# Kernel optimization log

Hardware: AMD Instinct MI355X
Metric: run time of the kernel (lower is better)

The kernel has to match this reference:

```python
import jax, jax.numpy as jnp
import numpy as np

THR = 0.2
BORDER_RM = 2
TEMP = 0.1


def _border_valid(n, b):
    idx = jnp.arange(n)
    return (idx >= b) & (idx < n - b)


def setup_inputs() -> dict:
    key = jax.random.key(0)
    k0, k1 = jax.random.split(key)
    N, L, S, C = 4, 3600, 3600, 256
    return {
        "feat_c0": jax.random.normal(k0, (N, L, C), dtype=jnp.float32),
        "feat_c1": jax.random.normal(k1, (N, S, C), dtype=jnp.float32),
        "h0c": 60, "w0c": 60, "h1c": 60, "w1c": 60,
    }


def reference(feat_c0, feat_c1, h0c, w0c, h1c, w1c):
    N, L, C = feat_c0.shape
    S = feat_c1.shape[1]
    inv_sqrt_c = 1.0 / (C ** 0.5)
    f0 = feat_c0 * inv_sqrt_c
    f1 = feat_c1 * inv_sqrt_c
    # [N, L, S] similarity, temperature 0.1
    sim = jnp.einsum('nlc,nsc->nls', f0, f1) / TEMP
    conf = jax.nn.softmax(sim, axis=1) * jax.nn.softmax(sim, axis=2)

    # threshold mask + border removal (applied in [b,h0,w0,h1,w1] layout,
    # expressed here as separable 1D validity masks -- same result, no 5D copy churn)
    v0h = _border_valid(h0c, BORDER_RM)  # [h0c]
    v0w = _border_valid(w0c, BORDER_RM)
    v1h = _border_valid(h1c, BORDER_RM)
    v1w = _border_valid(w1c, BORDER_RM)
    valid_l = (v0h[:, None] & v0w[None, :]).reshape(L)   # [L]
    valid_s = (v1h[:, None] & v1w[None, :]).reshape(S)   # [S]
    mask = (conf > THR) & valid_l[None, :, None] & valid_s[None, None, :]

    # mutual nearest (dual argmax equality)
    mask = mask & (conf == conf.max(axis=2, keepdims=True)) & (conf == conf.max(axis=1, keepdims=True))

    # fixed-shape match extraction: per (b, i) row, is there a match and where
    mask_v = jnp.any(mask, axis=2)                       # [N, L] bool
    all_j_ids = jnp.argmax(mask, axis=2)                 # [N, L] int
    mconf = jnp.take_along_axis(conf, all_j_ids[:, :, None], axis=2)[:, :, 0]
    mconf = jnp.where(mask_v, mconf, 0.0)                # [N, L]
    return conf, mask_v, all_j_ids, mconf
```

## Files before the change

### kernel.cpp

```cpp
#include <hip/hip_runtime.h>
#include <stdint.h>


typedef _Float16 f16;
typedef _Float16 f16x8 __attribute__((ext_vector_type(8)));
typedef _Float16 f16x4 __attribute__((ext_vector_type(4)));
typedef float f32x4 __attribute__((ext_vector_type(4)));

#define N_B 4
#define L_DIM 3600
#define S_DIM 3600
#define C_DIM 256

#define P1_THREADS 192
#define P1_BM 144
#define P1_BN 48
#define P1_ITERS 15
#define P1_CHUNK 720
#define P1_NCH 5
#define P1_NRT 25
#define YT_STRIDE 264

#define P2_ROWS 48
#define P2_NRT 75

#define C_EXP1 (0.0390625f * 1.4426950408889634f)

__global__ void cast_kernel(const float* __restrict__ a, const float* __restrict__ b,
                            f16* __restrict__ ah, f16* __restrict__ bh, int total8) {
  int i = blockIdx.x * blockDim.x + threadIdx.x;
  if (i >= total8) return;
  const float4* a4 = (const float4*)a;
  const float4* b4 = (const float4*)b;
  float4 x = a4[2 * (size_t)i], y = a4[2 * (size_t)i + 1];
  f16x8 o = {(f16)x.x, (f16)x.y, (f16)x.z, (f16)x.w,
             (f16)y.x, (f16)y.y, (f16)y.z, (f16)y.w};
  *(f16x8*)(ah + 8 * (size_t)i) = o;
  x = b4[2 * (size_t)i]; y = b4[2 * (size_t)i + 1];
  f16x8 o2 = {(f16)x.x, (f16)x.y, (f16)x.z, (f16)x.w,
              (f16)y.x, (f16)y.y, (f16)y.z, (f16)y.w};
  *(f16x8*)(bh + 8 * (size_t)i) = o2;
}

__global__ __launch_bounds__(P1_THREADS) void gemm_stats_kernel(
    const f16* __restrict__ X, const f16* __restrict__ Y,
    f16* __restrict__ eh, float* __restrict__ den_r, float* __restrict__ den_c) {
  __shared__ f16 Yt[P1_BN][YT_STRIDE];
  __shared__ float colsum_w[3][P1_CHUNK];
  const int rt = blockIdx.x, ch = blockIdx.y, n = blockIdx.z;
  const int tid = threadIdx.x;
  const int wave = tid >> 6, lane = tid & 63;
  const int q = lane >> 4, r = lane & 15;
  const int l0 = rt * P1_BM;
  const int s0 = ch * P1_CHUNK;

  f16x8 a[3][8];
#pragma unroll
  for (int grp = 0; grp < 3; ++grp) {
    const f16* xrow = X + ((size_t)n * L_DIM + l0 + wave * 48 + grp * 16 + r) * C_DIM;
#pragma unroll
    for (int k = 0; k < 8; ++k) a[grp][k] = *(const f16x8*)(xrow + k * 32 + q * 8);
  }

  float sum_e[3][4];
#pragma unroll
  for (int grp = 0; grp < 3; ++grp)
#pragma unroll
    for (int g = 0; g < 4; ++g) sum_e[grp][g] = 0.f;

  const f16* ebase = eh + ((size_t)n * L_DIM + l0 + wave * 48) * S_DIM;

  for (int it = 0; it < P1_ITERS; ++it) {
    const f16* ysrc = Y + ((size_t)n * S_DIM + s0 + it * P1_BN) * C_DIM;
#pragma unroll
    for (int i = 0; i < 8; ++i) {
      int c = i * P1_THREADS + tid;
      int row = c >> 5, cc = c & 31;
      *(f16x8*)&Yt[row][cc * 8] = *(const f16x8*)(ysrc + row * C_DIM + cc * 8);
    }
    __syncthreads();

    f32x4 acc[3][3];
#pragma unroll
    for (int grp = 0; grp < 3; ++grp)
#pragma unroll
      for (int nt = 0; nt < 3; ++nt) acc[grp][nt] = (f32x4){0.f, 0.f, 0.f, 0.f};

#pragma unroll
    for (int k = 0; k < 8; ++k) {
#pragma unroll
      for (int nt = 0; nt < 3; ++nt) {
        f16x8 b = *(const f16x8*)&Yt[nt * 16 + r][k * 32 + q * 8];
#pragma unroll
        for (int grp = 0; grp < 3; ++grp)
          acc[grp][nt] = __builtin_amdgcn_mfma_f32_16x16x32_f16(a[grp][k], b, acc[grp][nt], 0, 0, 0);
      }
    }
    __syncthreads();

#pragma unroll
    for (int nt = 0; nt < 3; ++nt) {
      int scol = s0 + it * P1_BN + nt * 16 + r;
      float csum = 0.f;
#pragma unroll
      for (int grp = 0; grp < 3; ++grp) {
#pragma unroll
        for (int g = 0; g < 4; ++g) {
          float e = exp2f(acc[grp][nt][g] * C_EXP1);
          sum_e[grp][g] += e;
          csum += e;
          ((f16*)ebase)[(size_t)(grp * 16 + q * 4 + g) * S_DIM + scol] = (f16)e;
        }
      }
      csum += __shfl_xor(csum, 16, 64);
      csum += __shfl_xor(csum, 32, 64);
      if (q == 0) colsum_w[wave][it * P1_BN + nt * 16 + r] = csum;
    }
  }

#pragma unroll
  for (int m = 1; m < 16; m <<= 1)
#pragma unroll
    for (int grp = 0; grp < 3; ++grp)
#pragma unroll
      for (int g = 0; g < 4; ++g) sum_e[grp][g] += __shfl_xor(sum_e[grp][g], m, 64);
  if (r == 0) {
#pragma unroll
    for (int grp = 0; grp < 3; ++grp)
#pragma unroll
      for (int g = 0; g < 4; ++g)
        atomicAdd(&den_r[n * L_DIM + l0 + wave * 48 + grp * 16 + q * 4 + g], sum_e[grp][g]);
  }

  __syncthreads();
  for (int i = tid; i < P1_CHUNK; i += P1_THREADS)
    atomicAdd(&den_c[n * S_DIM + s0 + i],
              colsum_w[0][i] + colsum_w[1][i] + colsum_w[2][i]);
}

__global__ void invert_kernel(float* __restrict__ a, float* __restrict__ b) {
  int i = blockIdx.x * blockDim.x + threadIdx.x;
  if (i >= N_B * L_DIM) return;
  a[i] = 1.0f / a[i];
  b[i] = 1.0f / b[i];
}

__global__ __launch_bounds__(256) void conf_kernel(
    const f16* __restrict__ eh, const float* __restrict__ invdr,
    const float* __restrict__ invdc, float* __restrict__ conf_out,
    unsigned long long* __restrict__ rowarg, float* __restrict__ colpart) {
  const int rt = blockIdx.x, n = blockIdx.y;
  const int tid = threadIdx.x;
  const int wave = tid >> 6, lane = tid & 63;
  const int l0 = rt * P2_ROWS;

  int colb[4];
  bool cv[4];
  float4 idc4[4];
  float4 cp[4];
#pragma unroll
  for (int ci = 0; ci < 4; ++ci) {
    int chunk = ci * 64 + lane;
    cv[ci] = chunk < 225;
    colb[ci] = (wave * 225 + (chunk < 225 ? chunk : 0)) * 4;
    idc4[ci] = *(const float4*)(invdc + n * S_DIM + colb[ci]);
    cp[ci] = (float4){0.f, 0.f, 0.f, 0.f};
  }

  for (int row = 0; row < P2_ROWS; ++row) {
    const int l = l0 + row;
    const f16* erow = eh + ((size_t)n * L_DIM + l) * S_DIM;
    float* crow = conf_out + ((size_t)n * L_DIM + l) * S_DIM;
    const float idr = invdr[n * L_DIM + l];
    float mx = 0.f;
    int mj = 0;
#pragma unroll
    for (int ci = 0; ci < 4; ++ci) {
      if (cv[ci]) {
        f16x4 e4 = *(const f16x4*)(erow + colb[ci]);
        float e0 = (float)e4.x, e1 = (float)e4.y, e2 = (float)e4.z, e3 = (float)e4.w;
        float4 w;
        w.x = e0 * e0 * idr * idc4[ci].x;
        w.y = e1 * e1 * idr * idc4[ci].y;
        w.z = e2 * e2 * idr * idc4[ci].z;
        w.w = e3 * e3 * idr * idc4[ci].w;
        *(float4*)(crow + colb[ci]) = w;
        int c0 = colb[ci];
        if (w.x > mx) { mx = w.x; mj = c0; }
        if (w.y > mx) { mx = w.y; mj = c0 + 1; }
        if (w.z > mx) { mx = w.z; mj = c0 + 2; }
        if (w.w > mx) { mx = w.w; mj = c0 + 3; }
        cp[ci].x = fmaxf(cp[ci].x, w.x);
        cp[ci].y = fmaxf(cp[ci].y, w.y);
        cp[ci].z = fmaxf(cp[ci].z, w.z);
        cp[ci].w = fmaxf(cp[ci].w, w.w);
      }
    }
#pragma unroll
    for (int m = 1; m < 64; m <<= 1) {
      float ov = __shfl_xor(mx, m, 64);
      int oj = __shfl_xor(mj, m, 64);
      if (ov > mx || (ov == mx && oj < mj)) { mx = ov; mj = oj; }
    }
    if (lane == 0) {
      unsigned long long key =
          ((unsigned long long)__float_as_uint(mx) << 32) |
          (unsigned int)(~(unsigned int)mj);
      atomicMax(&rowarg[n * L_DIM + l], key);
    }
  }

  float* cpo = colpart + ((size_t)n * P2_NRT + rt) * S_DIM;
#pragma unroll
  for (int ci = 0; ci < 4; ++ci)
    if (cv[ci]) *(float4*)(cpo + colb[ci]) = cp[ci];
}

__global__ void colmerge_kernel(const float* __restrict__ colpart,
                                float* __restrict__ colmax) {
  int i = blockIdx.x * blockDim.x + threadIdx.x;
  if (i >= N_B * S_DIM) return;
  int n = i / S_DIM, s = i - n * S_DIM;
  float m = 0.f;
  for (int rt = 0; rt < P2_NRT; ++rt)
    m = fmaxf(m, colpart[((size_t)n * P2_NRT + rt) * S_DIM + s]);
  colmax[i] = m;
}

__global__ void finalize_kernel(const unsigned long long* __restrict__ rowarg,
                                const float* __restrict__ colmax,
                                const int* __restrict__ h0c, const int* __restrict__ w0c,
                                const int* __restrict__ h1c, const int* __restrict__ w1c,
                                float* __restrict__ out_maskv, float* __restrict__ out_jids,
                                float* __restrict__ out_mconf) {
  int i = blockIdx.x * blockDim.x + threadIdx.x;
  if (i >= N_B * L_DIM) return;
  int n = i / L_DIM, l = i - n * L_DIM;
  unsigned long long key = rowarg[i];
  float rm = __uint_as_float((unsigned int)(key >> 32));
  int j = (int)(~(unsigned int)key);
  int W0 = *w0c, H0 = *h0c, W1 = *w1c, H1 = *h1c;
  int li = l / W0, lj = l - li * W0;
  bool vl = (li >= 2) && (li < H0 - 2) && (lj >= 2) && (lj < W0 - 2);
  int si = j / W1, sj = j - si * W1;
  bool vs = (si >= 2) && (si < H1 - 2) && (sj >= 2) && (sj < W1 - 2);
  float cm = colmax[n * S_DIM + j];
  bool mv = (rm > 0.2f) && vl && vs &&
            (__float_as_uint(rm) == __float_as_uint(cm));
  out_maskv[i] = mv ? 1.0f : 0.0f;
  out_jids[i]  = mv ? (float)j : 0.0f;
  out_mconf[i] = mv ? rm : 0.0f;
}

extern "C" void kernel_launch(void* const* d_in, const int* in_sizes, int n_in,
                              void* d_out, int out_size, void* d_ws, size_t ws_size,
                              hipStream_t stream) {
  const float* f0 = (const float*)d_in[0];
  const float* f1 = (const float*)d_in[1];
  const int* h0c = (const int*)d_in[2];
  const int* w0c = (const int*)d_in[3];
  const int* h1c = (const int*)d_in[4];
  const int* w1c = (const int*)d_in[5];

  char* ws = (char*)d_ws;
  size_t o = 0;
  f16* f0h = (f16*)(ws + o);               o += (size_t)N_B * L_DIM * C_DIM * 2;
  f16* f1h = (f16*)(ws + o);               o += (size_t)N_B * S_DIM * C_DIM * 2;
  float* den_r = (float*)(ws + o);         o += (size_t)N_B * L_DIM * 4;
  float* den_c = (float*)(ws + o);         o += (size_t)N_B * S_DIM * 4;
  unsigned long long* rowarg = (unsigned long long*)(ws + o); o += (size_t)N_B * L_DIM * 8;
  size_t zero_bytes = (size_t)N_B * L_DIM * (4 + 4 + 8);
  float* colmax = (float*)(ws + o);        o += (size_t)N_B * S_DIM * 4;
  float* colpart = (float*)(ws + o);       o += (size_t)N_B * P2_NRT * S_DIM * 4;
  f16* eh = (f16*)(ws + o);                o += (size_t)N_B * L_DIM * S_DIM * 2;

  float* conf = (float*)d_out;
  float* out_maskv = conf + (size_t)N_B * L_DIM * S_DIM;
  float* out_jids = out_maskv + N_B * L_DIM;
  float* out_mconf = out_jids + N_B * L_DIM;

  hipMemsetAsync(den_r, 0, zero_bytes, stream);

  int total8 = N_B * L_DIM * C_DIM / 8;
  cast_kernel<<<dim3((total8 + 255) / 256), 256, 0, stream>>>(f0, f1, f0h, f1h, total8);

  dim3 g1(P1_NRT, P1_NCH, N_B);
  gemm_stats_kernel<<<g1, P1_THREADS, 0, stream>>>(f0h, f1h, eh, den_r, den_c);
  invert_kernel<<<(N_B * L_DIM + 255) / 256, 256, 0, stream>>>(den_r, den_c);
  dim3 g2(P2_NRT, N_B);
  conf_kernel<<<g2, 256, 0, stream>>>(eh, den_r, den_c, conf, rowarg, colpart);
  colmerge_kernel<<<(N_B * S_DIM + 255) / 256, 256, 0, stream>>>(colpart, colmax);
  finalize_kernel<<<(N_B * L_DIM + 255) / 256, 256, 0, stream>>>(
      rowarg, colmax, h0c, w0c, h1c, w1c, out_maskv, out_jids, out_mconf);
}
```

Baseline: 416.7 us.

## Recompute GEMM in conf pass instead of storing fp16 exp matrix

```diff
diff --git a/kernel.cpp b/kernel.cpp
--- a/kernel.cpp
+++ b/kernel.cpp
@@ -4,7 +4,6 @@
 
 typedef _Float16 f16;
 typedef _Float16 f16x8 __attribute__((ext_vector_type(8)));
-typedef _Float16 f16x4 __attribute__((ext_vector_type(4)));
 typedef float f32x4 __attribute__((ext_vector_type(4)));
 
 #define N_B 4
@@ -21,10 +20,8 @@
 #define P1_NRT 25
 #define YT_STRIDE 264
 
-#define P2_ROWS 48
-#define P2_NRT 75
-
 #define C_EXP1 (0.0390625f * 1.4426950408889634f)
+#define C_EXP2 (0.0781250f * 1.4426950408889634f)
 
 __global__ void cast_kernel(const float* __restrict__ a, const float* __restrict__ b,
                             f16* __restrict__ ah, f16* __restrict__ bh, int total8) {
@@ -44,7 +41,7 @@
 
 __global__ __launch_bounds__(P1_THREADS) void gemm_stats_kernel(
     const f16* __restrict__ X, const f16* __restrict__ Y,
-    f16* __restrict__ eh, float* __restrict__ den_r, float* __restrict__ den_c) {
+    float* __restrict__ den_r, float* __restrict__ den_c) {
   __shared__ f16 Yt[P1_BN][YT_STRIDE];
   __shared__ float colsum_w[3][P1_CHUNK];
   const int rt = blockIdx.x, ch = blockIdx.y, n = blockIdx.z;
@@ -68,8 +65,6 @@
 #pragma unroll
     for (int g = 0; g < 4; ++g) sum_e[grp][g] = 0.f;
 
-  const f16* ebase = eh + ((size_t)n * L_DIM + l0 + wave * 48) * S_DIM;
-
   for (int it = 0; it < P1_ITERS; ++it) {
     const f16* ysrc = Y + ((size_t)n * S_DIM + s0 + it * P1_BN) * C_DIM;
 #pragma unroll
@@ -100,7 +95,6 @@
 
 #pragma unroll
     for (int nt = 0; nt < 3; ++nt) {
-      int scol = s0 + it * P1_BN + nt * 16 + r;
       float csum = 0.f;
 #pragma unroll
       for (int grp = 0; grp < 3; ++grp) {
@@ -109,7 +103,6 @@
           float e = exp2f(acc[grp][nt][g] * C_EXP1);
           sum_e[grp][g] += e;
           csum += e;
-          ((f16*)ebase)[(size_t)(grp * 16 + q * 4 + g) * S_DIM + scol] = (f16)e;
         }
       }
       csum += __shfl_xor(csum, 16, 64);
@@ -145,86 +138,121 @@
   b[i] = 1.0f / b[i];
 }
 
-__global__ __launch_bounds__(256) void conf_kernel(
-    const f16* __restrict__ eh, const float* __restrict__ invdr,
-    const float* __restrict__ invdc, float* __restrict__ conf_out,
-    unsigned long long* __restrict__ rowarg, float* __restrict__ colpart) {
-  const int rt = blockIdx.x, n = blockIdx.y;
+__global__ __launch_bounds__(P1_THREADS) void gemm_conf_kernel(
+    const f16* __restrict__ X, const f16* __restrict__ Y,
+    const float* __restrict__ invdr, const float* __restrict__ invdc,
+    float* __restrict__ conf_out,
+    unsigned long long* __restrict__ rowarg,
+    unsigned int* __restrict__ colmax_bits) {
+  __shared__ f16 Yt[P1_BN][YT_STRIDE];
+  __shared__ float colmax_w[3][P1_CHUNK];
+  const int rt = blockIdx.x, ch = blockIdx.y, n = blockIdx.z;
   const int tid = threadIdx.x;
   const int wave = tid >> 6, lane = tid & 63;
-  const int l0 = rt * P2_ROWS;
-
-  int colb[4];
-  bool cv[4];
-  float4 idc4[4];
-  float4 cp[4];
-#pragma unroll
-  for (int ci = 0; ci < 4; ++ci) {
-    int chunk = ci * 64 + lane;
-    cv[ci] = chunk < 225;
-    colb[ci] = (wave * 225 + (chunk < 225 ? chunk : 0)) * 4;
-    idc4[ci] = *(const float4*)(invdc + n * S_DIM + colb[ci]);
-    cp[ci] = (float4){0.f, 0.f, 0.f, 0.f};
-  }
-
-  for (int row = 0; row < P2_ROWS; ++row) {
-    const int l = l0 + row;
-    const f16* erow = eh + ((size_t)n * L_DIM + l) * S_DIM;
-    float* crow = conf_out + ((size_t)n * L_DIM + l) * S_DIM;
-    const float idr = invdr[n * L_DIM + l];
-    float mx = 0.f;
-    int mj = 0;
-#pragma unroll
-    for (int ci = 0; ci < 4; ++ci) {
-      if (cv[ci]) {
-        f16x4 e4 = *(const f16x4*)(erow + colb[ci]);
-        float e0 = (float)e4.x, e1 = (float)e4.y, e2 = (float)e4.z, e3 = (float)e4.w;
-        float4 w;
-        w.x = e0 * e0 * idr * idc4[ci].x;
-        w.y = e1 * e1 * idr * idc4[ci].y;
-        w.z = e2 * e2 * idr * idc4[ci].z;
-        w.w = e3 * e3 * idr * idc4[ci].w;
-        *(float4*)(crow + colb[ci]) = w;
-        int c0 = colb[ci];
-        if (w.x > mx) { mx = w.x; mj = c0; }
-        if (w.y > mx) { mx = w.y; mj = c0 + 1; }
-        if (w.z > mx) { mx = w.z; mj = c0 + 2; }
-        if (w.w > mx) { mx = w.w; mj = c0 + 3; }
-        cp[ci].x = fmaxf(cp[ci].x, w.x);
-        cp[ci].y = fmaxf(cp[ci].y, w.y);
-        cp[ci].z = fmaxf(cp[ci].z, w.z);
-        cp[ci].w = fmaxf(cp[ci].w, w.w);
-      }
-    }
-#pragma unroll
-    for (int m = 1; m < 64; m <<= 1) {
-      float ov = __shfl_xor(mx, m, 64);
-      int oj = __shfl_xor(mj, m, 64);
-      if (ov > mx || (ov == mx && oj < mj)) { mx = ov; mj = oj; }
-    }
-    if (lane == 0) {
-      unsigned long long key =
-          ((unsigned long long)__float_as_uint(mx) << 32) |
-          (unsigned int)(~(unsigned int)mj);
-      atomicMax(&rowarg[n * L_DIM + l], key);
-    }
-  }
-
-  float* cpo = colpart + ((size_t)n * P2_NRT + rt) * S_DIM;
-#pragma unroll
-  for (int ci = 0; ci < 4; ++ci)
-    if (cv[ci]) *(float4*)(cpo + colb[ci]) = cp[ci];
-}
-
-__global__ void colmerge_kernel(const float* __restrict__ colpart,
-                                float* __restrict__ colmax) {
-  int i = blockIdx.x * blockDim.x + threadIdx.x;
-  if (i >= N_B * S_DIM) return;
-  int n = i / S_DIM, s = i - n * S_DIM;
-  float m = 0.f;
-  for (int rt = 0; rt < P2_NRT; ++rt)
-    m = fmaxf(m, colpart[((size_t)n * P2_NRT + rt) * S_DIM + s]);
-  colmax[i] = m;
+  const int q = lane >> 4, r = lane & 15;
+  const int l0 = rt * P1_BM;
+  const int s0 = ch * P1_CHUNK;
+
+  f16x8 a[3][8];
+#pragma unroll
+  for (int grp = 0; grp < 3; ++grp) {
+    const f16* xrow = X + ((size_t)n * L_DIM + l0 + wave * 48 + grp * 16 + r) * C_DIM;
+#pragma unroll
+    for (int k = 0; k < 8; ++k) a[grp][k] = *(const f16x8*)(xrow + k * 32 + q * 8);
+  }
+
+  float idr[3][4];
+#pragma unroll
+  for (int grp = 0; grp < 3; ++grp)
+#pragma unroll
+    for (int g = 0; g < 4; ++g)
+      idr[grp][g] = invdr[n * L_DIM + l0 + wave * 48 + grp * 16 + q * 4 + g];
+
+  float mx[12];
+  int mj[12];
+#pragma unroll
+  for (int i = 0; i < 12; ++i) { mx[i] = 0.f; mj[i] = 0; }
+
+  float* cbase = conf_out + ((size_t)n * L_DIM + l0 + wave * 48) * S_DIM;
+
+  for (int it = 0; it < P1_ITERS; ++it) {
+    const f16* ysrc = Y + ((size_t)n * S_DIM + s0 + it * P1_BN) * C_DIM;
+#pragma unroll
+    for (int i = 0; i < 8; ++i) {
+      int c = i * P1_THREADS + tid;
+      int row = c >> 5, cc = c & 31;
+      *(f16x8*)&Yt[row][cc * 8] = *(const f16x8*)(ysrc + row * C_DIM + cc * 8);
+    }
+    __syncthreads();
+
+    f32x4 acc[3][3];
+#pragma unroll
+    for (int grp = 0; grp < 3; ++grp)
+#pragma unroll
+      for (int nt = 0; nt < 3; ++nt) acc[grp][nt] = (f32x4){0.f, 0.f, 0.f, 0.f};
+
+#pragma unroll
+    for (int k = 0; k < 8; ++k) {
+#pragma unroll
+      for (int nt = 0; nt < 3; ++nt) {
+        f16x8 b = *(const f16x8*)&Yt[nt * 16 + r][k * 32 + q * 8];
+#pragma unroll
+        for (int grp = 0; grp < 3; ++grp)
+          acc[grp][nt] = __builtin_amdgcn_mfma_f32_16x16x32_f16(a[grp][k], b, acc[grp][nt], 0, 0, 0);
+      }
+    }
+    __syncthreads();
+
+#pragma unroll
+    for (int nt = 0; nt < 3; ++nt) {
+      const int scol = s0 + it * P1_BN + nt * 16 + r;
+      const float idc = invdc[n * S_DIM + scol];
+      float cm = 0.f;
+#pragma unroll
+      for (int grp = 0; grp < 3; ++grp) {
+#pragma unroll
+        for (int g = 0; g < 4; ++g) {
+          float w = exp2f(acc[grp][nt][g] * C_EXP2) * idr[grp][g] * idc;
+          cbase[(size_t)(grp * 16 + q * 4 + g) * S_DIM + scol] = w;
+          const int idx = grp * 4 + g;
+          if (w > mx[idx]) { mx[idx] = w; mj[idx] = scol; }
+          cm = fmaxf(cm, w);
+        }
+      }
+      cm = fmaxf(cm, __shfl_xor(cm, 16, 64));
+      cm = fmaxf(cm, __shfl_xor(cm, 32, 64));
+      if (q == 0) colmax_w[wave][it * P1_BN + nt * 16 + r] = cm;
+    }
+  }
+
+#pragma unroll
+  for (int m = 1; m < 16; m <<= 1) {
+#pragma unroll
+    for (int idx = 0; idx < 12; ++idx) {
+      float ov = __shfl_xor(mx[idx], m, 64);
+      int oj = __shfl_xor(mj[idx], m, 64);
+      if (ov > mx[idx] || (ov == mx[idx] && oj < mj[idx])) { mx[idx] = ov; mj[idx] = oj; }
+    }
+  }
+  if (r == 0) {
+#pragma unroll
+    for (int grp = 0; grp < 3; ++grp) {
+#pragma unroll
+      for (int g = 0; g < 4; ++g) {
+        const int idx = grp * 4 + g;
+        unsigned long long key =
+            ((unsigned long long)__float_as_uint(mx[idx]) << 32) |
+            (unsigned int)(~(unsigned int)mj[idx]);
+        atomicMax(&rowarg[n * L_DIM + l0 + wave * 48 + grp * 16 + q * 4 + g], key);
+      }
+    }
+  }
+
+  __syncthreads();
+  for (int i = tid; i < P1_CHUNK; i += P1_THREADS) {
+    float m3 = fmaxf(fmaxf(colmax_w[0][i], colmax_w[1][i]), colmax_w[2][i]);
+    atomicMax(&colmax_bits[n * S_DIM + s0 + i], __float_as_uint(m3));
+  }
 }
 
 __global__ void finalize_kernel(const unsigned long long* __restrict__ rowarg,
@@ -269,10 +297,8 @@
   float* den_r = (float*)(ws + o);         o += (size_t)N_B * L_DIM * 4;
   float* den_c = (float*)(ws + o);         o += (size_t)N_B * S_DIM * 4;
   unsigned long long* rowarg = (unsigned long long*)(ws + o); o += (size_t)N_B * L_DIM * 8;
-  size_t zero_bytes = (size_t)N_B * L_DIM * (4 + 4 + 8);
   float* colmax = (float*)(ws + o);        o += (size_t)N_B * S_DIM * 4;
-  float* colpart = (float*)(ws + o);       o += (size_t)N_B * P2_NRT * S_DIM * 4;
-  f16* eh = (f16*)(ws + o);                o += (size_t)N_B * L_DIM * S_DIM * 2;
+  size_t zero_bytes = (size_t)N_B * (L_DIM * 4 + S_DIM * 4 + L_DIM * 8 + S_DIM * 4);
 
   float* conf = (float*)d_out;
   float* out_maskv = conf + (size_t)N_B * L_DIM * S_DIM;
@@ -285,11 +311,10 @@
   cast_kernel<<<dim3((total8 + 255) / 256), 256, 0, stream>>>(f0, f1, f0h, f1h, total8);
 
   dim3 g1(P1_NRT, P1_NCH, N_B);
-  gemm_stats_kernel<<<g1, P1_THREADS, 0, stream>>>(f0h, f1h, eh, den_r, den_c);
+  gemm_stats_kernel<<<g1, P1_THREADS, 0, stream>>>(f0h, f1h, den_r, den_c);
   invert_kernel<<<(N_B * L_DIM + 255) / 256, 256, 0, stream>>>(den_r, den_c);
-  dim3 g2(P2_NRT, N_B);
-  conf_kernel<<<g2, 256, 0, stream>>>(eh, den_r, den_c, conf, rowarg, colpart);
-  colmerge_kernel<<<(N_B * S_DIM + 255) / 256, 256, 0, stream>>>(colpart, colmax);
+  gemm_conf_kernel<<<g1, P1_THREADS, 0, stream>>>(
+      f0h, f1h, den_r, den_c, conf, rowarg, (unsigned int*)colmax);
   finalize_kernel<<<(N_B * L_DIM + 255) / 256, 256, 0, stream>>>(
       rowarg, colmax, h0c, w0c, h1c, w1c, out_maskv, out_jids, out_mconf);
 }
```

Measured after the change: 431.5 us. 1.04x slower.

## Transpose MFMA output for vector e stores and stream conf with LDS column max

Applied to the files above, without the earlier changes.

```diff
diff --git a/kernel.cpp b/kernel.cpp
--- a/kernel.cpp
+++ b/kernel.cpp
@@ -15,14 +15,13 @@
 #define P1_THREADS 192
 #define P1_BM 144
 #define P1_BN 48
-#define P1_ITERS 15
-#define P1_CHUNK 720
-#define P1_NCH 5
+#define P1_ITERS 5
+#define P1_CHUNK 240
+#define P1_NCH 15
 #define P1_NRT 25
 #define YT_STRIDE 264
 
-#define P2_ROWS 48
-#define P2_NRT 75
+#define PB_ROWS 16
 
 #define C_EXP1 (0.0390625f * 1.4426950408889634f)
 
@@ -42,11 +41,11 @@
   *(f16x8*)(bh + 8 * (size_t)i) = o2;
 }
 
-__global__ __launch_bounds__(P1_THREADS) void gemm_stats_kernel(
+__global__ __launch_bounds__(P1_THREADS, 2) void gemm_stats_e_kernel(
     const f16* __restrict__ X, const f16* __restrict__ Y,
     f16* __restrict__ eh, float* __restrict__ den_r, float* __restrict__ den_c) {
   __shared__ f16 Yt[P1_BN][YT_STRIDE];
-  __shared__ float colsum_w[3][P1_CHUNK];
+  __shared__ __attribute__((aligned(16))) float colsum_w[3][P1_CHUNK];
   const int rt = blockIdx.x, ch = blockIdx.y, n = blockIdx.z;
   const int tid = threadIdx.x;
   const int wave = tid >> 6, lane = tid & 63;
@@ -62,13 +61,11 @@
     for (int k = 0; k < 8; ++k) a[grp][k] = *(const f16x8*)(xrow + k * 32 + q * 8);
   }
 
-  float sum_e[3][4];
-#pragma unroll
-  for (int grp = 0; grp < 3; ++grp)
-#pragma unroll
-    for (int g = 0; g < 4; ++g) sum_e[grp][g] = 0.f;
-
-  const f16* ebase = eh + ((size_t)n * L_DIM + l0 + wave * 48) * S_DIM;
+  float prs[3];
+#pragma unroll
+  for (int grp = 0; grp < 3; ++grp) prs[grp] = 0.f;
+
+  f16* ebase = eh + ((size_t)n * L_DIM + l0 + wave * 48) * S_DIM;
 
   for (int it = 0; it < P1_ITERS; ++it) {
     const f16* ysrc = Y + ((size_t)n * S_DIM + s0 + it * P1_BN) * C_DIM;
@@ -93,43 +90,46 @@
         f16x8 b = *(const f16x8*)&Yt[nt * 16 + r][k * 32 + q * 8];
 #pragma unroll
         for (int grp = 0; grp < 3; ++grp)
-          acc[grp][nt] = __builtin_amdgcn_mfma_f32_16x16x32_f16(a[grp][k], b, acc[grp][nt], 0, 0, 0);
+          acc[grp][nt] = __builtin_amdgcn_mfma_f32_16x16x32_f16(b, a[grp][k], acc[grp][nt], 0, 0, 0);
       }
     }
     __syncthreads();
 
 #pragma unroll
     for (int nt = 0; nt < 3; ++nt) {
-      int scol = s0 + it * P1_BN + nt * 16 + r;
-      float csum = 0.f;
+      const int sl = it * P1_BN + nt * 16 + q * 4;
+      f32x4 c4 = (f32x4){0.f, 0.f, 0.f, 0.f};
 #pragma unroll
       for (int grp = 0; grp < 3; ++grp) {
-#pragma unroll
-        for (int g = 0; g < 4; ++g) {
-          float e = exp2f(acc[grp][nt][g] * C_EXP1);
-          sum_e[grp][g] += e;
-          csum += e;
-          ((f16*)ebase)[(size_t)(grp * 16 + q * 4 + g) * S_DIM + scol] = (f16)e;
-        }
-      }
-      csum += __shfl_xor(csum, 16, 64);
-      csum += __shfl_xor(csum, 32, 64);
-      if (q == 0) colsum_w[wave][it * P1_BN + nt * 16 + r] = csum;
-    }
-  }
-
-#pragma unroll
-  for (int m = 1; m < 16; m <<= 1)
+        f32x4 e4;
+        e4.x = exp2f(acc[grp][nt][0] * C_EXP1);
+        e4.y = exp2f(acc[grp][nt][1] * C_EXP1);
+        e4.z = exp2f(acc[grp][nt][2] * C_EXP1);
+        e4.w = exp2f(acc[grp][nt][3] * C_EXP1);
+        f16x4 h = {(f16)e4.x, (f16)e4.y, (f16)e4.z, (f16)e4.w};
+        *(f16x4*)(ebase + (size_t)(grp * 16 + r) * S_DIM + s0 + sl) = h;
+        prs[grp] += e4.x + e4.y + e4.z + e4.w;
+        c4.x += e4.x; c4.y += e4.y; c4.z += e4.z; c4.w += e4.w;
+      }
+#pragma unroll
+      for (int m = 1; m < 16; m <<= 1) {
+        c4.x += __shfl_xor(c4.x, m, 64);
+        c4.y += __shfl_xor(c4.y, m, 64);
+        c4.z += __shfl_xor(c4.z, m, 64);
+        c4.w += __shfl_xor(c4.w, m, 64);
+      }
+      if (r == 0) *(f32x4*)&colsum_w[wave][sl] = c4;
+    }
+  }
+
+#pragma unroll
+  for (int m = 16; m < 64; m <<= 1)
+#pragma unroll
+    for (int grp = 0; grp < 3; ++grp) prs[grp] += __shfl_xor(prs[grp], m, 64);
+  if (q == 0) {
 #pragma unroll
     for (int grp = 0; grp < 3; ++grp)
-#pragma unroll
-      for (int g = 0; g < 4; ++g) sum_e[grp][g] += __shfl_xor(sum_e[grp][g], m, 64);
-  if (r == 0) {
-#pragma unroll
-    for (int grp = 0; grp < 3; ++grp)
-#pragma unroll
-      for (int g = 0; g < 4; ++g)
-        atomicAdd(&den_r[n * L_DIM + l0 + wave * 48 + grp * 16 + q * 4 + g], sum_e[grp][g]);
+      atomicAdd(&den_r[n * L_DIM + l0 + wave * 48 + grp * 16 + r], prs[grp]);
   }
 
   __syncthreads();
@@ -145,55 +145,52 @@
   b[i] = 1.0f / b[i];
 }
 
-__global__ __launch_bounds__(256) void conf_kernel(
+__global__ __launch_bounds__(256, 4) void conf_stream_kernel(
     const f16* __restrict__ eh, const float* __restrict__ invdr,
     const float* __restrict__ invdc, float* __restrict__ conf_out,
-    unsigned long long* __restrict__ rowarg, float* __restrict__ colpart) {
-  const int rt = blockIdx.x, n = blockIdx.y;
-  const int tid = threadIdx.x;
-  const int wave = tid >> 6, lane = tid & 63;
-  const int l0 = rt * P2_ROWS;
-
-  int colb[4];
-  bool cv[4];
-  float4 idc4[4];
-  float4 cp[4];
-#pragma unroll
-  for (int ci = 0; ci < 4; ++ci) {
-    int chunk = ci * 64 + lane;
-    cv[ci] = chunk < 225;
-    colb[ci] = (wave * 225 + (chunk < 225 ? chunk : 0)) * 4;
-    idc4[ci] = *(const float4*)(invdc + n * S_DIM + colb[ci]);
-    cp[ci] = (float4){0.f, 0.f, 0.f, 0.f};
-  }
-
-  for (int row = 0; row < P2_ROWS; ++row) {
-    const int l = l0 + row;
+    unsigned long long* __restrict__ rowarg,
+    unsigned int* __restrict__ colmax_bits) {
+  __shared__ unsigned cmx_lds[S_DIM];
+  const int n = blockIdx.y;
+  const int l0 = blockIdx.x * PB_ROWS;
+  const int tid = threadIdx.x, wave = tid >> 6, lane = tid & 63;
+
+  for (int i = tid; i < S_DIM; i += 256) cmx_lds[i] = 0u;
+  __syncthreads();
+
+  f32x4 cm[15];
+#pragma unroll
+  for (int c = 0; c < 15; ++c) cm[c] = (f32x4){0.f, 0.f, 0.f, 0.f};
+
+  const float* idcb = invdc + (size_t)n * S_DIM;
+
+  for (int rr = 0; rr < 4; ++rr) {
+    const int l = l0 + wave * 4 + rr;
+    const float idr = invdr[n * L_DIM + l];
     const f16* erow = eh + ((size_t)n * L_DIM + l) * S_DIM;
     float* crow = conf_out + ((size_t)n * L_DIM + l) * S_DIM;
-    const float idr = invdr[n * L_DIM + l];
     float mx = 0.f;
     int mj = 0;
 #pragma unroll
-    for (int ci = 0; ci < 4; ++ci) {
-      if (cv[ci]) {
-        f16x4 e4 = *(const f16x4*)(erow + colb[ci]);
-        float e0 = (float)e4.x, e1 = (float)e4.y, e2 = (float)e4.z, e3 = (float)e4.w;
-        float4 w;
-        w.x = e0 * e0 * idr * idc4[ci].x;
-        w.y = e1 * e1 * idr * idc4[ci].y;
-        w.z = e2 * e2 * idr * idc4[ci].z;
-        w.w = e3 * e3 * idr * idc4[ci].w;
-        *(float4*)(crow + colb[ci]) = w;
-        int c0 = colb[ci];
-        if (w.x > mx) { mx = w.x; mj = c0; }
-        if (w.y > mx) { mx = w.y; mj = c0 + 1; }
-        if (w.z > mx) { mx = w.z; mj = c0 + 2; }
-        if (w.w > mx) { mx = w.w; mj = c0 + 3; }
-        cp[ci].x = fmaxf(cp[ci].x, w.x);
-        cp[ci].y = fmaxf(cp[ci].y, w.y);
-        cp[ci].z = fmaxf(cp[ci].z, w.z);
-        cp[ci].w = fmaxf(cp[ci].w, w.w);
+    for (int c = 0; c < 15; ++c) {
+      if (c < 14 || lane < 4) {
+        const int col = c * 256 + lane * 4;
+        f16x4 e4 = *(const f16x4*)(erow + col);
+        const float4 idc4 = *(const float4*)(idcb + col);
+        f32x4 w;
+        w.x = (float)e4.x * (float)e4.x * idr * idc4.x;
+        w.y = (float)e4.y * (float)e4.y * idr * idc4.y;
+        w.z = (float)e4.z * (float)e4.z * idr * idc4.z;
+        w.w = (float)e4.w * (float)e4.w * idr * idc4.w;
+        __builtin_nontemporal_store(w, (f32x4*)(crow + col));
+        if (w.x > mx) { mx = w.x; mj = col; }
+        if (w.y > mx) { mx = w.y; mj = col + 1; }
+        if (w.z > mx) { mx = w.z; mj = col + 2; }
+        if (w.w > mx) { mx = w.w; mj = col + 3; }
+        cm[c].x = fmaxf(cm[c].x, w.x);
+        cm[c].y = fmaxf(cm[c].y, w.y);
+        cm[c].z = fmaxf(cm[c].z, w.z);
+        cm[c].w = fmaxf(cm[c].w, w.w);
       }
     }
 #pragma unroll
@@ -206,25 +203,23 @@
       unsigned long long key =
           ((unsigned long long)__float_as_uint(mx) << 32) |
           (unsigned int)(~(unsigned int)mj);
-      atomicMax(&rowarg[n * L_DIM + l], key);
-    }
-  }
-
-  float* cpo = colpart + ((size_t)n * P2_NRT + rt) * S_DIM;
-#pragma unroll
-  for (int ci = 0; ci < 4; ++ci)
-    if (cv[ci]) *(float4*)(cpo + colb[ci]) = cp[ci];
-}
-
-__global__ void colmerge_kernel(const float* __restrict__ colpart,
-                                float* __restrict__ colmax) {
-  int i = blockIdx.x * blockDim.x + threadIdx.x;
-  if (i >= N_B * S_DIM) return;
-  int n = i / S_DIM, s = i - n * S_DIM;
-  float m = 0.f;
-  for (int rt = 0; rt < P2_NRT; ++rt)
-    m = fmaxf(m, colpart[((size_t)n * P2_NRT + rt) * S_DIM + s]);
-  colmax[i] = m;
+      rowarg[n * L_DIM + l] = key;
+    }
+  }
+
+#pragma unroll
+  for (int c = 0; c < 15; ++c) {
+    if (c < 14 || lane < 4) {
+      const int col = c * 256 + lane * 4;
+      atomicMax(&cmx_lds[col + 0], __float_as_uint(cm[c].x));
+      atomicMax(&cmx_lds[col + 1], __float_as_uint(cm[c].y));
+      atomicMax(&cmx_lds[col + 2], __float_as_uint(cm[c].z));
+      atomicMax(&cmx_lds[col + 3], __float_as_uint(cm[c].w));
+    }
+  }
+  __syncthreads();
+  for (int i = tid; i < S_DIM; i += 256)
+    atomicMax(&colmax_bits[(size_t)n * S_DIM + i], cmx_lds[i]);
 }
 
 __global__ void finalize_kernel(const unsigned long long* __restrict__ rowarg,
@@ -268,10 +263,9 @@
   f16* f1h = (f16*)(ws + o);               o += (size_t)N_B * S_DIM * C_DIM * 2;
   float* den_r = (float*)(ws + o);         o += (size_t)N_B * L_DIM * 4;
   float* den_c = (float*)(ws + o);         o += (size_t)N_B * S_DIM * 4;
+  float* colmax = (float*)(ws + o);        o += (size_t)N_B * S_DIM * 4;
+  size_t zero_bytes = (size_t)N_B * (L_DIM * 4 + S_DIM * 4 + S_DIM * 4);
   unsigned long long* rowarg = (unsigned long long*)(ws + o); o += (size_t)N_B * L_DIM * 8;
-  size_t zero_bytes = (size_t)N_B * L_DIM * (4 + 4 + 8);
-  float* colmax = (float*)(ws + o);        o += (size_t)N_B * S_DIM * 4;
-  float* colpart = (float*)(ws + o);       o += (size_t)N_B * P2_NRT * S_DIM * 4;
   f16* eh = (f16*)(ws + o);                o += (size_t)N_B * L_DIM * S_DIM * 2;
 
   float* conf = (float*)d_out;
@@ -285,11 +279,11 @@
   cast_kernel<<<dim3((total8 + 255) / 256), 256, 0, stream>>>(f0, f1, f0h, f1h, total8);
 
   dim3 g1(P1_NRT, P1_NCH, N_B);
-  gemm_stats_kernel<<<g1, P1_THREADS, 0, stream>>>(f0h, f1h, eh, den_r, den_c);
+  gemm_stats_e_kernel<<<g1, P1_THREADS, 0, stream>>>(f0h, f1h, eh, den_r, den_c);
   invert_kernel<<<(N_B * L_DIM + 255) / 256, 256, 0, stream>>>(den_r, den_c);
-  dim3 g2(P2_NRT, N_B);
-  conf_kernel<<<g2, 256, 0, stream>>>(eh, den_r, den_c, conf, rowarg, colpart);
-  colmerge_kernel<<<(N_B * S_DIM + 255) / 256, 256, 0, stream>>>(colpart, colmax);
+  dim3 g2(L_DIM / PB_ROWS, N_B);
+  conf_stream_kernel<<<g2, 256, 0, stream>>>(
+      eh, den_r, den_c, conf, rowarg, (unsigned int*)colmax);
   finalize_kernel<<<(N_B * L_DIM + 255) / 256, 256, 0, stream>>>(
       rowarg, colmax, h0c, w0c, h1c, w1c, out_maskv, out_jids, out_mconf);
 }
```

New measurement: 517.2 us. 1.24x slower.
